# Optimization experiments

Measured on AMD Instinct MI355X. Metric: run time of the kernel, lower is better.

Reference implementation:

```python
import jax, jax.numpy as jnp
import numpy as np

Q = 10000   # num_question
D = 64      # dim_s
M = 50      # size_m
B = 64      # batch
T = 512     # seq_len


def setup_inputs() -> dict:
    key = jax.random.key(0)
    ks = jax.random.split(key, 14)
    s = 1.0 / np.sqrt(D)
    inp = {
        "question": jax.random.randint(ks[0], (B, T), 0, Q, dtype=jnp.int32),
        "response": jax.random.randint(ks[1], (B, T), 0, 2, dtype=jnp.int32),
        "mask": jnp.ones((B, T), dtype=jnp.float32),
        "k_emb": jax.random.normal(ks[2], (Q, D), jnp.float32) * s,
        "v_emb": jax.random.normal(ks[3], (2 * Q, D), jnp.float32) * s,
        "Mk": jax.random.normal(ks[4], (M, D), jnp.float32) * np.sqrt(2.0 / D),
        "Mv0": jax.random.normal(ks[5], (M, D), jnp.float32) * np.sqrt(2.0 / D),
        "e_W": jax.random.normal(ks[6], (D, D), jnp.float32) * s,
        "e_b": jnp.zeros((D,), jnp.float32),
        "a_W": jax.random.normal(ks[7], (D, D), jnp.float32) * s,
        "a_b": jnp.zeros((D,), jnp.float32),
        "f_W": jax.random.normal(ks[8], (2 * D, D), jnp.float32) * (1.0 / np.sqrt(2 * D)),
        "f_b": jnp.zeros((D,), jnp.float32),
        "p_W": jax.random.normal(ks[9], (D, 1), jnp.float32) * s,
        "p_b": jnp.zeros((1,), jnp.float32),
    }
    return inp


def reference(question, response, mask, k_emb, v_emb, Mk, Mv0,
              e_W, e_b, a_W, a_b, f_W, f_b, p_W, p_b):
    num_q = k_emb.shape[0]
    bsz = question.shape[0]
    x = question + num_q * response                      # [B,T] combined ids
    k = k_emb[question]                                  # [B,T,D]
    v = v_emb[x]                                         # [B,T,D]
    w = jax.nn.softmax(k @ Mk.T, axis=-1)                # [B,T,M] read/write weights
    e = jax.nn.sigmoid(v @ e_W + e_b)                    # [B,T,D] erase
    a = jnp.tanh(v @ a_W + a_b)                          # [B,T,D] add

    def step(Mvt, inp):
        wt, et, at, mt = inp                             # [B,M],[B,D],[B,D],[B]
        Mvn = Mvt * (1.0 - wt[:, :, None] * et[:, None, :]) + wt[:, :, None] * at[:, None, :]
        Mvt = jnp.where(mt[:, None, None] == 1, Mvn, Mvt)
        return Mvt, Mvt

    Mv0b = jnp.broadcast_to(Mv0, (bsz,) + Mv0.shape)     # [B,M,D]
    xs = (jnp.swapaxes(w, 0, 1), jnp.swapaxes(e, 0, 1),
          jnp.swapaxes(a, 0, 1), mask.T)
    _, Mv_seq = jax.lax.scan(step, Mv0b, xs)             # [T,B,M,D] states after steps 0..T-1
    # read at step t (t>=1) uses state after step t-1
    Mv_read = jnp.swapaxes(Mv_seq[:-1], 0, 1)            # [B,T-1,M,D]
    read = jnp.einsum('btm,btmd->btd', w[:, 1:], Mv_read)
    f = jnp.tanh(jnp.concatenate([read, k[:, 1:]], axis=-1) @ f_W + f_b)
    p = (f @ p_W + p_b).squeeze(-1)                      # [B,T-1]
    return p
```

## Files before the change

kernel.cpp:

```cpp
#include <hip/hip_runtime.h>
#include <cstddef>

#define QN 10000
#define DD 64
#define MM 50
#define BB 64
#define TT 512
#define WPAD 52
#define MG 25

#define PIN(arr, n)                                        \
  _Pragma("unroll") for (int _p = 0; _p < (n); ++_p)       \
      asm volatile("" : "+v"((arr)[_p]));

__global__ __launch_bounds__(256) void kPre(
    const int* __restrict__ question, const int* __restrict__ response,
    const float* __restrict__ mask,
    const float* __restrict__ k_emb, const float* __restrict__ v_emb,
    const float* __restrict__ Mk,
    const float* __restrict__ e_W, const float* __restrict__ e_b,
    const float* __restrict__ a_W, const float* __restrict__ a_b,
    float* __restrict__ w_buf, float* __restrict__ e_buf,
    float* __restrict__ a_buf) {
  const int lane = (int)(threadIdx.x & 63);
  const int wslot = __builtin_amdgcn_readfirstlane((int)(threadIdx.x >> 6));
  const int gw = blockIdx.x * 4 + wslot;
  const int NW = gridDim.x * 4;
  const int wq = (NW * 2) / 5;
  const int eq = (NW * 3) / 10;
  const int aq = NW - wq - eq;

  if (gw < wq) {
    const int idx = gw;
    const int stride4 = wq * 4;
    float mk[64];
    const int mrow = lane < MM ? lane : (MM - 1);
#pragma unroll
    for (int i = 0; i < 64; i += 4) {
      const float4 t4 = *(const float4*)(Mk + mrow * 64 + i);
      mk[i] = t4.x; mk[i + 1] = t4.y; mk[i + 2] = t4.z; mk[i + 3] = t4.w;
    }
    for (int base = idx * 4; base < BB * TT; base += stride4) {
      const int4 q4 = *(const int4*)(question + base);
      const float* __restrict__ kr0 = k_emb + (size_t)q4.x * 64;
      const float* __restrict__ kr1 = k_emb + (size_t)q4.y * 64;
      const float* __restrict__ kr2 = k_emb + (size_t)q4.z * 64;
      const float* __restrict__ kr3 = k_emb + (size_t)q4.w * 64;
      float l00=0.f,l01=0.f,l02=0.f,l03=0.f;
      float l10=0.f,l11=0.f,l12=0.f,l13=0.f;
      float l20=0.f,l21=0.f,l22=0.f,l23=0.f;
      float l30=0.f,l31=0.f,l32=0.f,l33=0.f;
#pragma unroll
      for (int i = 0; i < 64; i += 4) {
        const float4 k0 = *(const float4*)(kr0 + i);
        const float4 k1 = *(const float4*)(kr1 + i);
        const float4 k2 = *(const float4*)(kr2 + i);
        const float4 k3 = *(const float4*)(kr3 + i);
        l00 = fmaf(k0.x, mk[i], l00); l01 = fmaf(k0.y, mk[i+1], l01);
        l02 = fmaf(k0.z, mk[i+2], l02); l03 = fmaf(k0.w, mk[i+3], l03);
        l10 = fmaf(k1.x, mk[i], l10); l11 = fmaf(k1.y, mk[i+1], l11);
        l12 = fmaf(k1.z, mk[i+2], l12); l13 = fmaf(k1.w, mk[i+3], l13);
        l20 = fmaf(k2.x, mk[i], l20); l21 = fmaf(k2.y, mk[i+1], l21);
        l22 = fmaf(k2.z, mk[i+2], l22); l23 = fmaf(k2.w, mk[i+3], l23);
        l30 = fmaf(k3.x, mk[i], l30); l31 = fmaf(k3.y, mk[i+1], l31);
        l32 = fmaf(k3.z, mk[i+2], l32); l33 = fmaf(k3.w, mk[i+3], l33);
      }
      float lm[4];
      lm[0] = (l00 + l01) + (l02 + l03);
      lm[1] = (l10 + l11) + (l12 + l13);
      lm[2] = (l20 + l21) + (l22 + l23);
      lm[3] = (l30 + l31) + (l32 + l33);
#pragma unroll
      for (int r = 0; r < 4; ++r) {
        float lv = (lane < MM) ? lm[r] : -3.4e38f;
#pragma unroll
        for (int off = 32; off > 0; off >>= 1) lv = fmaxf(lv, __shfl_xor(lv, off));
        float pe = (lane < MM) ? __expf(lm[r] - lv) : 0.f;
        float ss = pe;
#pragma unroll
        for (int off = 32; off > 0; off >>= 1) ss += __shfl_xor(ss, off);
        if (lane < MM) w_buf[(size_t)(base + r) * WPAD + lane] = pe / ss;
      }
    }
  } else if (gw < wq + eq) {
    const int idx = gw - wq;
    const int stride4 = eq * 4;
    float ew[64];
#pragma unroll
    for (int i = 0; i < 64; ++i) ew[i] = e_W[i * 64 + lane];
    const float eb = e_b[lane];
    for (int base = idx * 4; base < BB * TT; base += stride4) {
      const int4 q4 = *(const int4*)(question + base);
      const int4 r4 = *(const int4*)(response + base);
      const float4 m4 = *(const float4*)(mask + base);
      const float* __restrict__ v0 = v_emb + ((size_t)q4.x + (size_t)QN * r4.x) * 64;
      const float* __restrict__ v1 = v_emb + ((size_t)q4.y + (size_t)QN * r4.y) * 64;
      const float* __restrict__ v2 = v_emb + ((size_t)q4.z + (size_t)QN * r4.z) * 64;
      const float* __restrict__ v3 = v_emb + ((size_t)q4.w + (size_t)QN * r4.w) * 64;
      float e00 = eb, e01 = 0.f, e10 = eb, e11 = 0.f;
      float e20 = eb, e21 = 0.f, e30 = eb, e31 = 0.f;
#pragma unroll
      for (int i = 0; i < 64; i += 4) {
        const float4 a0 = *(const float4*)(v0 + i);
        const float4 a1 = *(const float4*)(v1 + i);
        const float4 a2 = *(const float4*)(v2 + i);
        const float4 a3 = *(const float4*)(v3 + i);
        e00 = fmaf(a0.x, ew[i], e00);     e01 = fmaf(a0.y, ew[i + 1], e01);
        e00 = fmaf(a0.z, ew[i + 2], e00); e01 = fmaf(a0.w, ew[i + 3], e01);
        e10 = fmaf(a1.x, ew[i], e10);     e11 = fmaf(a1.y, ew[i + 1], e11);
        e10 = fmaf(a1.z, ew[i + 2], e10); e11 = fmaf(a1.w, ew[i + 3], e11);
        e20 = fmaf(a2.x, ew[i], e20);     e21 = fmaf(a2.y, ew[i + 1], e21);
        e20 = fmaf(a2.z, ew[i + 2], e20); e21 = fmaf(a2.w, ew[i + 3], e21);
        e30 = fmaf(a3.x, ew[i], e30);     e31 = fmaf(a3.y, ew[i + 1], e31);
        e30 = fmaf(a3.z, ew[i + 2], e30); e31 = fmaf(a3.w, ew[i + 3], e31);
      }
      const float mf0 = (m4.x == 1.0f) ? 1.0f : 0.0f;
      const float mf1 = (m4.y == 1.0f) ? 1.0f : 0.0f;
      const float mf2 = (m4.z == 1.0f) ? 1.0f : 0.0f;
      const float mf3 = (m4.w == 1.0f) ? 1.0f : 0.0f;
      e_buf[(size_t)(base + 0) * 64 + lane] = mf0 / (1.f + __expf(-(e00 + e01)));
      e_buf[(size_t)(base + 1) * 64 + lane] = mf1 / (1.f + __expf(-(e10 + e11)));
      e_buf[(size_t)(base + 2) * 64 + lane] = mf2 / (1.f + __expf(-(e20 + e21)));
      e_buf[(size_t)(base + 3) * 64 + lane] = mf3 / (1.f + __expf(-(e30 + e31)));
    }
  } else {
    const int idx = gw - wq - eq;
    const int stride4 = aq * 4;
    float aw[64];
#pragma unroll
    for (int i = 0; i < 64; ++i) aw[i] = a_W[i * 64 + lane];
    const float ab = a_b[lane];
    for (int base = idx * 4; base < BB * TT; base += stride4) {
      const int4 q4 = *(const int4*)(question + base);
      const int4 r4 = *(const int4*)(response + base);
      const float4 m4 = *(const float4*)(mask + base);
      const float* __restrict__ v0 = v_emb + ((size_t)q4.x + (size_t)QN * r4.x) * 64;
      const float* __restrict__ v1 = v_emb + ((size_t)q4.y + (size_t)QN * r4.y) * 64;
      const float* __restrict__ v2 = v_emb + ((size_t)q4.z + (size_t)QN * r4.z) * 64;
      const float* __restrict__ v3 = v_emb + ((size_t)q4.w + (size_t)QN * r4.w) * 64;
      float a00 = ab, a01 = 0.f, a10 = ab, a11 = 0.f;
      float a20 = ab, a21 = 0.f, a30 = ab, a31 = 0.f;
#pragma unroll
      for (int i = 0; i < 64; i += 4) {
        const float4 x0 = *(const float4*)(v0 + i);
        const float4 x1 = *(const float4*)(v1 + i);
        const float4 x2 = *(const float4*)(v2 + i);
        const float4 x3 = *(const float4*)(v3 + i);
        a00 = fmaf(x0.x, aw[i], a00);     a01 = fmaf(x0.y, aw[i + 1], a01);
        a00 = fmaf(x0.z, aw[i + 2], a00); a01 = fmaf(x0.w, aw[i + 3], a01);
        a10 = fmaf(x1.x, aw[i], a10);     a11 = fmaf(x1.y, aw[i + 1], a11);
        a10 = fmaf(x1.z, aw[i + 2], a10); a11 = fmaf(x1.w, aw[i + 3], a11);
        a20 = fmaf(x2.x, aw[i], a20);     a21 = fmaf(x2.y, aw[i + 1], a21);
        a20 = fmaf(x2.z, aw[i + 2], a20); a21 = fmaf(x2.w, aw[i + 3], a21);
        a30 = fmaf(x3.x, aw[i], a30);     a31 = fmaf(x3.y, aw[i + 1], a31);
        a30 = fmaf(x3.z, aw[i + 2], a30); a31 = fmaf(x3.w, aw[i + 3], a31);
      }
      const float mf0 = (m4.x == 1.0f) ? 1.0f : 0.0f;
      const float mf1 = (m4.y == 1.0f) ? 1.0f : 0.0f;
      const float mf2 = (m4.z == 1.0f) ? 1.0f : 0.0f;
      const float mf3 = (m4.w == 1.0f) ? 1.0f : 0.0f;
      const float s0 = a00 + a01, s1 = a10 + a11, s2 = a20 + a21, s3 = a30 + a31;
      a_buf[(size_t)(base + 0) * 64 + lane] = mf0 * (1.f - 2.f / (__expf(2.f * s0) + 1.f));
      a_buf[(size_t)(base + 1) * 64 + lane] = mf1 * (1.f - 2.f / (__expf(2.f * s1) + 1.f));
      a_buf[(size_t)(base + 2) * 64 + lane] = mf2 * (1.f - 2.f / (__expf(2.f * s2) + 1.f));
      a_buf[(size_t)(base + 3) * 64 + lane] = mf3 * (1.f - 2.f / (__expf(2.f * s3) + 1.f));
    }
  }
}

#define STAGE_W(wl_row, rowbase)                                            \
  {                                                                         \
    const float* __restrict__ wsrc = w_buf + (rowbase) * WPAD;              \
    _Pragma("unroll") for (int k = 0; k < 13; ++k) {                        \
      const int idx = lane + k * 64;                            \
      const int row = idx / 52;                                             \
      const int col = idx - row * 52;                                       \
      (wl_row)[row * 56 + col + (col >= 25 ? 3 : 0)] = wsrc[idx];           \
    }                                                                       \
  }

#define LOAD_WM(wm, wl_row, j, g)                                           \
  const float* __restrict__ wj_##j = (wl_row) + (j) * 56 + (g) * 28;        \
  const float4 q0_##j = *(const float4*)(wj_##j + 0);                       \
  const float4 q1_##j = *(const float4*)(wj_##j + 4);                       \
  const float4 q2_##j = *(const float4*)(wj_##j + 8);                       \
  const float4 q3_##j = *(const float4*)(wj_##j + 12);                      \
  const float4 q4_##j = *(const float4*)(wj_##j + 16);                      \
  const float4 q5_##j = *(const float4*)(wj_##j + 20);                      \
  const float4 q6_##j = *(const float4*)(wj_##j + 24);                      \
  const float wm[MG] = {q0_##j.x, q0_##j.y, q0_##j.z, q0_##j.w,             \
                        q1_##j.x, q1_##j.y, q1_##j.z, q1_##j.w,             \
                        q2_##j.x, q2_##j.y, q2_##j.z, q2_##j.w,             \
                        q3_##j.x, q3_##j.y, q3_##j.z, q3_##j.w,             \
                        q4_##j.x, q4_##j.y, q4_##j.z, q4_##j.w,             \
                        q5_##j.x, q5_##j.y, q5_##j.z, q5_##j.w, q6_##j.x};

__global__ __launch_bounds__(256) void kA16(
    const float* __restrict__ w_buf, const float* __restrict__ e_buf,
    const float* __restrict__ a_buf, float* __restrict__ AB) {
  __shared__ float wl[4][16 * 56];
  const int lane = (int)(threadIdx.x & 63);
  const int wslot = __builtin_amdgcn_readfirstlane((int)(threadIdx.x >> 6));
  const int u2 = blockIdx.x * 4 + wslot;
  if (u2 >= BB * 32 * 2) return;
  const int g = u2 & 1;
  const int unit = u2 >> 1;
  const int b = unit >> 5;
  const int c = unit & 31;
  const size_t rowbase = (size_t)b * TT + c * 16;
  const size_t eb0 = rowbase * 64 + lane;

  float ev[16], av[16];
#pragma unroll
  for (int j = 0; j < 16; ++j) {
    ev[j] = e_buf[eb0 + (size_t)j * 64];
    av[j] = a_buf[eb0 + (size_t)j * 64];
  }
  STAGE_W(wl[wslot], rowbase)

  float Am[MG], Bm[MG];
#pragma unroll
  for (int m = 0; m < MG; ++m) { Am[m] = 1.f; Bm[m] = 0.f; }

#pragma unroll
  for (int j = 0; j < 16; ++j) {
    LOAD_WM(wm, wl[wslot], j, g)
#pragma unroll
    for (int m = 0; m < MG; ++m) {
      const float al = fmaf(-wm[m], ev[j], 1.0f);
      const float be = wm[m] * av[j];
      Am[m] *= al;
      Bm[m] = fmaf(Bm[m], al, be);
    }
  }
  float* __restrict__ abp = AB + (size_t)unit * 6400 + (g * MG) * 128 + lane * 2;
#pragma unroll
  for (int m = 0; m < MG; ++m) {
    float2 o; o.x = Am[m]; o.y = Bm[m];
    *(float2*)(abp + m * 128) = o;
  }
}

__global__ __launch_bounds__(256) void kB_entry(
    const float* __restrict__ AB, const float* __restrict__ Mv0,
    float* __restrict__ entry, int C) {
  const int NT = gridDim.x * 256;
  for (int idx = blockIdx.x * 256 + (int)threadIdx.x; idx < BB * MM * 64;
       idx += NT) {
    const int b = idx / (MM * 64);
    const int r = idx - b * (MM * 64);
    float s = Mv0[r];
    const float* __restrict__ abp = AB + (size_t)b * C * 6400 + (size_t)r * 2;
    float* __restrict__ ep = entry + (size_t)b * C * 3200 + r;
    if (C == 32) {
      float2 ab[32];
#pragma unroll
      for (int c = 0; c < 32; ++c)
        ab[c] = *(const float2*)(abp + (size_t)c * 6400);
#pragma unroll
      for (int c = 0; c < 32; ++c) {
        ep[(size_t)c * 3200] = s;
        s = fmaf(ab[c].x, s, ab[c].y);
      }
    } else {
      float2 cur = *(const float2*)(abp);
      for (int c = 0; c < C; ++c) {
        ep[(size_t)c * 3200] = s;
        float2 nxt; nxt.x = 1.f; nxt.y = 0.f;
        if (c + 1 < C) nxt = *(const float2*)(abp + (size_t)(c + 1) * 6400);
        s = fmaf(cur.x, s, cur.y);
        cur = nxt;
      }
    }
  }
}

__global__ __launch_bounds__(256) void kC16sum(
    const float* __restrict__ w_buf, const float* __restrict__ e_buf,
    const float* __restrict__ a_buf, const float* __restrict__ entry,
    float* __restrict__ read_buf) {
  __shared__ float wl[4][16 * 56];
  __shared__ float p_lds[4][16][64];
  const int lane = (int)(threadIdx.x & 63);
  const int wslot = __builtin_amdgcn_readfirstlane((int)(threadIdx.x >> 6));
  const int u2 = blockIdx.x * 4 + wslot;
  const int g = u2 & 1;
  const int unit = u2 >> 1;
  const int b = unit >> 5;
  const int c = unit & 31;
  const size_t rowbase = (size_t)b * TT + c * 16;
  const size_t eb0 = rowbase * 64 + lane;

  float ev[16], av[16];
#pragma unroll
  for (int j = 0; j < 16; ++j) {
    ev[j] = e_buf[eb0 + (size_t)j * 64];
    av[j] = a_buf[eb0 + (size_t)j * 64];
  }
  float s[MG];
  {
    const float* __restrict__ ep =
        entry + (size_t)unit * 3200 + (g * MG) * 64 + lane;
#pragma unroll
    for (int m = 0; m < MG; ++m) s[m] = ep[m * 64];
  }
  STAGE_W(wl[wslot], rowbase)

#pragma unroll
  for (int j = 0; j < 16; ++j) {
    LOAD_WM(wm, wl[wslot], j, g)
    float a0 = 0.f, a1 = 0.f;
#pragma unroll
    for (int m = 0; m < MG - 1; m += 2) {
      a0 = fmaf(wm[m], s[m], a0);
      a1 = fmaf(wm[m + 1], s[m + 1], a1);
    }
    a0 = fmaf(wm[MG - 1], s[MG - 1], a0);
    p_lds[wslot][j][lane] = a0 + a1;
#pragma unroll
    for (int m = 0; m < MG; ++m)
      s[m] = fmaf(wm[m], fmaf(-s[m], ev[j], av[j]), s[m]);
  }
  __syncthreads();

  {
    const int p = wslot >> 1;
    const int uown = blockIdx.x * 2 + p;
    const int ob = uown >> 5;
    const int oc = uown & 31;
    const int t0 = oc * 16;
    const int j0 = (oc == 0 && g == 0) ? 1 : g * 8;
    const int j1 = g * 8 + 8;
    for (int j = j0; j < j1; ++j) {
      const int t = t0 + j;
      const float r = p_lds[2 * p][j][lane] + p_lds[2 * p + 1][j][lane];
      read_buf[((size_t)ob * (TT - 1) + (t - 1)) * 64 + lane] = r;
    }
  }
}

__global__ __launch_bounds__(256) void kA_chunk(
    const float* __restrict__ w_buf, const float* __restrict__ e_buf,
    const float* __restrict__ a_buf, float* __restrict__ AB, int logC, int L) {
  const int lane = (int)(threadIdx.x & 63);
  const int wslot = __builtin_amdgcn_readfirstlane((int)(threadIdx.x >> 6));
  const int NW = gridDim.x * 4;
  const int C = 1 << logC;
  for (int u2 = blockIdx.x * 4 + wslot; u2 < BB * C * 2; u2 += NW) {
    const int g = u2 & 1;
    const int unit = u2 >> 1;
    const int b = unit >> logC;
    const int c = unit & (C - 1);
    float Am[MG], Bm[MG];
#pragma unroll
    for (int m = 0; m < MG; ++m) { Am[m] = 1.f; Bm[m] = 0.f; }
    const size_t rowbase = (size_t)b * TT + c * L;
#pragma unroll 2
    for (int j = 0; j < L; ++j) {
      const size_t row = rowbase + j;
      const float ed = e_buf[row * 64 + lane];
      const float ad = a_buf[row * 64 + lane];
      const float* __restrict__ wr = w_buf + row * WPAD + g * MG;
#pragma unroll
      for (int m = 0; m < MG; ++m) {
        const float wm = wr[m];
        const float al = fmaf(-wm, ed, 1.0f);
        const float be = wm * ad;
        Am[m] *= al;
        Bm[m] = fmaf(Bm[m], al, be);
      }
    }
    float* __restrict__ abp = AB + (size_t)unit * 6400 + (g * MG) * 128 + lane * 2;
#pragma unroll
    for (int m = 0; m < MG; ++m) {
      float2 o; o.x = Am[m]; o.y = Bm[m];
      *(float2*)(abp + m * 128) = o;
    }
  }
}

__global__ __launch_bounds__(256) void kC_read(
    const float* __restrict__ w_buf, const float* __restrict__ e_buf,
    const float* __restrict__ a_buf, const float* __restrict__ entry,
    const float* __restrict__ Mv0, float* __restrict__ read2,
    int logC, int L, int use_mv0) {
  const int lane = (int)(threadIdx.x & 63);
  const int wslot = __builtin_amdgcn_readfirstlane((int)(threadIdx.x >> 6));
  const int NW = gridDim.x * 4;
  const int C = 1 << logC;
  const size_t RN = (size_t)BB * (TT - 1) * 64;
  for (int u2 = blockIdx.x * 4 + wslot; u2 < BB * C * 2; u2 += NW) {
    const int g = u2 & 1;
    const int unit = u2 >> 1;
    const int b = unit >> logC;
    const int c = unit & (C - 1);
    float s[MG];
    if (use_mv0) {
#pragma unroll
      for (int m = 0; m < MG; ++m) s[m] = Mv0[(g * MG + m) * 64 + lane];
    } else {
      const float* __restrict__ ep =
          entry + (size_t)unit * 3200 + (g * MG) * 64 + lane;
#pragma unroll
      for (int m = 0; m < MG; ++m) s[m] = ep[m * 64];
    }
    const int t0 = c * L;
    float* __restrict__ rb = read2 + (size_t)g * RN;
    for (int j = 0; j < L; ++j) {
      const int t = t0 + j;
      const size_t row = (size_t)b * TT + t;
      const float ed = e_buf[row * 64 + lane];
      const float ad = a_buf[row * 64 + lane];
      const float* __restrict__ wr = w_buf + row * WPAD + g * MG;
      if (t >= 1) {
        float a0 = 0.f, a1 = 0.f;
#pragma unroll
        for (int m = 0; m < MG - 1; m += 2) {
          a0 = fmaf(wr[m], s[m], a0);
          a1 = fmaf(wr[m + 1], s[m + 1], a1);
        }
        a0 = fmaf(wr[MG - 1], s[MG - 1], a0);
        rb[((size_t)b * (TT - 1) + (t - 1)) * 64 + lane] = a0 + a1;
      }
#pragma unroll
      for (int m = 0; m < MG; ++m)
        s[m] = fmaf(wr[m], fmaf(-s[m], ed, ad), s[m]);
    }
  }
}

__global__ __launch_bounds__(256) void k3_out(
    const int* __restrict__ question, const float* __restrict__ k_emb,
    const float* __restrict__ read_buf,
    const float* __restrict__ f_W, const float* __restrict__ f_b,
    const float* __restrict__ p_W, const float* __restrict__ p_b,
    float* __restrict__ out) {
  __shared__ float pbuf[2][2][64];
  __shared__ float stg[4][64];
  const int lane = (int)(threadIdx.x & 63);
  const int ws = __builtin_amdgcn_readfirstlane((int)(threadIdx.x >> 6));
  const int pair = ws >> 1;
  const int g = ws & 1;
  const int NP = gridDim.x * 2;
  const int R = BB * (TT - 1);
  const int iters = (R + NP - 1) / NP;

  float fw[64];
#pragma unroll
  for (int i = 0; i < 64; ++i) fw[i] = f_W[(g * 64 + i) * 64 + lane];
  PIN(fw, 64)
  const float fb = f_b[lane];
  const float pw = p_W[lane];
  const float pb = p_b[0];

  int row = blockIdx.x * 2 + pair;
  float cur = 0.f;
  if (row < R) {
    if (g == 0) {
      cur = read_buf[(size_t)row * 64 + lane];
    } else {
      const int b = row / (TT - 1);
      const int tp = row - b * (TT - 1);
      const int qn = question[b * TT + tp + 1];
      cur = k_emb[(size_t)qn * 64 + lane];
    }
  }
  for (int it = 0; it < iters; ++it) {
    const int nrow = row + NP;
    float nxt = 0.f;
    if (nrow < R) {
      if (g == 0) {
        nxt = read_buf[(size_t)nrow * 64 + lane];
      } else {
        const int nb = nrow / (TT - 1);
        const int ntp = nrow - nb * (TT - 1);
        const int nqn = question[nb * TT + ntp + 1];
        nxt = k_emb[(size_t)nqn * 64 + lane];
      }
    }
    const bool active = (row < R);
    float partial = 0.f;
    if (active) {
      stg[ws][lane] = cur;
      float f0 = (g == 0) ? fb : 0.f, f1 = 0.f, f2 = 0.f, f3 = 0.f;
#pragma unroll
      for (int i = 0; i < 64; i += 4) {
        const float4 xv = *(const float4*)&stg[ws][i];
        f0 = fmaf(xv.x, fw[i], f0);
        f1 = fmaf(xv.y, fw[i + 1], f1);
        f2 = fmaf(xv.z, fw[i + 2], f2);
        f3 = fmaf(xv.w, fw[i + 3], f3);
      }
      partial = (f0 + f1) + (f2 + f3);
    }
    const int pr = it & 1;
    if (active && g == 1) pbuf[pr][pair][lane] = partial;
    __syncthreads();
    if (active && g == 0) {
      const float f = partial + pbuf[pr][pair][lane];
      const float t2 = __expf(2.f * f);
      const float fv = 1.f - 2.f / (t2 + 1.f);
      float acc = fv * pw;
#pragma unroll
      for (int off = 32; off > 0; off >>= 1) acc += __shfl_xor(acc, off);
      if (lane == 0) out[row] = acc + pb;
    }
    row = nrow; cur = nxt;
  }
}

__global__ __launch_bounds__(256) void k3_out2(
    const int* __restrict__ question, const float* __restrict__ k_emb,
    const float* __restrict__ read2,
    const float* __restrict__ f_W, const float* __restrict__ f_b,
    const float* __restrict__ p_W, const float* __restrict__ p_b,
    float* __restrict__ out) {
  __shared__ float pbuf[2][2][64];
  __shared__ float stg[4][64];
  const int lane = (int)(threadIdx.x & 63);
  const int ws = __builtin_amdgcn_readfirstlane((int)(threadIdx.x >> 6));
  const int pair = ws >> 1;
  const int g = ws & 1;
  const int NP = gridDim.x * 2;
  const size_t RN = (size_t)BB * (TT - 1) * 64;
  const int R = BB * (TT - 1);
  const int iters = (R + NP - 1) / NP;

  float fw[64];
#pragma unroll
  for (int i = 0; i < 64; ++i) fw[i] = f_W[(g * 64 + i) * 64 + lane];
  PIN(fw, 64)
  const float fb = f_b[lane];
  const float pw = p_W[lane];
  const float pb = p_b[0];

  int row = blockIdx.x * 2 + pair;
  float cur = 0.f;
  if (row < R) {
    if (g == 0) {
      cur = read2[(size_t)row * 64 + lane] + read2[RN + (size_t)row * 64 + lane];
    } else {
      const int b = row / (TT - 1);
      const int tp = row - b * (TT - 1);
      const int qn = question[b * TT + tp + 1];
      cur = k_emb[(size_t)qn * 64 + lane];
    }
  }
  for (int it = 0; it < iters; ++it) {
    const int nrow = row + NP;
    float nxt = 0.f;
    if (nrow < R) {
      if (g == 0) {
        nxt = read2[(size_t)nrow * 64 + lane] +
              read2[RN + (size_t)nrow * 64 + lane];
      } else {
        const int nb = nrow / (TT - 1);
        const int ntp = nrow - nb * (TT - 1);
        const int nqn = question[nb * TT + ntp + 1];
        nxt = k_emb[(size_t)nqn * 64 + lane];
      }
    }
    const bool active = (row < R);
    float partial = 0.f;
    if (active) {
      stg[ws][lane] = cur;
      float f0 = (g == 0) ? fb : 0.f, f1 = 0.f, f2 = 0.f, f3 = 0.f;
#pragma unroll
      for (int i = 0; i < 64; i += 4) {
        const float4 xv = *(const float4*)&stg[ws][i];
        f0 = fmaf(xv.x, fw[i], f0);
        f1 = fmaf(xv.y, fw[i + 1], f1);
        f2 = fmaf(xv.z, fw[i + 2], f2);
        f3 = fmaf(xv.w, fw[i + 3], f3);
      }
      partial = (f0 + f1) + (f2 + f3);
    }
    const int pr = it & 1;
    if (active && g == 1) pbuf[pr][pair][lane] = partial;
    __syncthreads();
    if (active && g == 0) {
      const float f = partial + pbuf[pr][pair][lane];
      const float t2 = __expf(2.f * f);
      const float fv = 1.f - 2.f / (t2 + 1.f);
      float acc = fv * pw;
#pragma unroll
      for (int off = 32; off > 0; off >>= 1) acc += __shfl_xor(acc, off);
      if (lane == 0) out[row] = acc + pb;
    }
    row = nrow; cur = nxt;
  }
}

extern "C" void kernel_launch(void* const* d_in, const int* in_sizes, int n_in,
                              void* d_out, int out_size, void* d_ws, size_t ws_size,
                              hipStream_t stream) {
  const int*   question = (const int*)d_in[0];
  const int*   response = (const int*)d_in[1];
  const float* mask     = (const float*)d_in[2];
  const float* k_emb    = (const float*)d_in[3];
  const float* v_emb    = (const float*)d_in[4];
  const float* Mk       = (const float*)d_in[5];
  const float* Mv0      = (const float*)d_in[6];
  const float* e_W      = (const float*)d_in[7];
  const float* e_b      = (const float*)d_in[8];
  const float* a_W      = (const float*)d_in[9];
  const float* a_b      = (const float*)d_in[10];
  const float* f_W      = (const float*)d_in[11];
  const float* f_b      = (const float*)d_in[12];
  const float* p_W      = (const float*)d_in[13];
  const float* p_b      = (const float*)d_in[14];
  float* out = (float*)d_out;

  const size_t wN  = (size_t)BB * TT * WPAD;
  const size_t eN  = (size_t)BB * TT * 64;
  const size_t r2N = 2ull * BB * (TT - 1) * 64;
  float* ws = (float*)d_ws;
  float* w_buf  = ws;
  float* e_buf  = w_buf + wN;
  float* a_buf  = e_buf + eN;
  float* readws = a_buf + eN;
  float* AB_arr = readws + r2N;
  const size_t baseN = wN + 2 * eN + r2N;

  int C = 32, logC = 5;
  while (C >= 2) {
    const size_t need = (baseN + 9600ull * BB * C) * sizeof(float);
    if (need <= ws_size) break;
    C >>= 1; logC -= 1;
  }
  int useChunks = (C >= 2);
  if (!useChunks) { C = 1; logC = 0; }
  const int L = TT / C;
  float* entry = AB_arr + 6400ull * BB * C;

  hipLaunchKernelGGL(kPre, dim3(2048), dim3(256), 0, stream,
                     question, response, mask, k_emb, v_emb, Mk,
                     e_W, e_b, a_W, a_b, w_buf, e_buf, a_buf);

  if (C == 32) {
    hipLaunchKernelGGL(kA16, dim3(1024), dim3(256), 0, stream,
                       w_buf, e_buf, a_buf, AB_arr);
    hipLaunchKernelGGL(kB_entry, dim3((BB * MM * 64 + 255) / 256), dim3(256),
                       0, stream, AB_arr, Mv0, entry, C);
    hipLaunchKernelGGL(kC16sum, dim3(1024), dim3(256), 0, stream,
                       w_buf, e_buf, a_buf, entry, readws);
    hipLaunchKernelGGL(k3_out, dim3(1024), dim3(256), 0, stream,
                       question, k_emb, readws, f_W, f_b, p_W, p_b, out);
  } else {
    if (useChunks) {
      const int ublocksA = (BB * C * 2 + 3) / 4;
      hipLaunchKernelGGL(kA_chunk, dim3(ublocksA), dim3(256), 0, stream,
                         w_buf, e_buf, a_buf, AB_arr, logC, L);
      hipLaunchKernelGGL(kB_entry, dim3((BB * MM * 64 + 255) / 256), dim3(256),
                         0, stream, AB_arr, Mv0, entry, C);
    }
    const int ublocksC = (BB * C * 2 + 3) / 4;
    hipLaunchKernelGGL(kC_read, dim3(ublocksC), dim3(256), 0, stream,
                       w_buf, e_buf, a_buf, entry, Mv0, readws,
                       logC, L, useChunks ? 0 : 1);
    hipLaunchKernelGGL(k3_out2, dim3(1024), dim3(256), 0, stream,
                       question, k_emb, readws, f_W, f_b, p_W, p_b, out);
  }
}
```

Measured before the change: 181.2 us.

## Fuse chunk read kernel with output projection to drop read buffer round-trip

Merges the per-chunk memory-read kernel and the output MLP kernel into one kernel for the C==32 path. Read vectors stay in LDS and feed the f_W/p_W projection directly, so the read buffer is never written to or read back from global memory, and one kernel launch is removed. In exchange, each block now loads the 64-register f_W slice and runs 16 serialized steps with a block barrier each, which raises register pressure and may lower occupancy.

```diff
diff --git a/kernel.cpp b/kernel.cpp
--- a/kernel.cpp
+++ b/kernel.cpp
@@ -275,12 +275,18 @@
   }
 }
 
-__global__ __launch_bounds__(256) void kC16sum(
+__global__ __launch_bounds__(256) void kCD2(
+    const int* __restrict__ question,
     const float* __restrict__ w_buf, const float* __restrict__ e_buf,
     const float* __restrict__ a_buf, const float* __restrict__ entry,
-    float* __restrict__ read_buf) {
+    const float* __restrict__ k_emb,
+    const float* __restrict__ f_W, const float* __restrict__ f_b,
+    const float* __restrict__ p_W, const float* __restrict__ p_b,
+    float* __restrict__ out) {
   __shared__ float wl[4][16 * 56];
   __shared__ float p_lds[4][16][64];
+  __shared__ float pbuf[2][2][64];
+  __shared__ float stg[4][64];
   const int lane = (int)(threadIdx.x & 63);
   const int wslot = __builtin_amdgcn_readfirstlane((int)(threadIdx.x >> 6));
   const int u2 = blockIdx.x * 4 + wslot;
@@ -291,50 +297,91 @@
   const size_t rowbase = (size_t)b * TT + c * 16;
   const size_t eb0 = rowbase * 64 + lane;
 
-  float ev[16], av[16];
-#pragma unroll
-  for (int j = 0; j < 16; ++j) {
-    ev[j] = e_buf[eb0 + (size_t)j * 64];
-    av[j] = a_buf[eb0 + (size_t)j * 64];
-  }
-  float s[MG];
   {
+    float ev[16], av[16];
+#pragma unroll
+    for (int j = 0; j < 16; ++j) {
+      ev[j] = e_buf[eb0 + (size_t)j * 64];
+      av[j] = a_buf[eb0 + (size_t)j * 64];
+    }
+    float s[MG];
     const float* __restrict__ ep =
         entry + (size_t)unit * 3200 + (g * MG) * 64 + lane;
 #pragma unroll
     for (int m = 0; m < MG; ++m) s[m] = ep[m * 64];
-  }
-  STAGE_W(wl[wslot], rowbase)
-
-#pragma unroll
+    STAGE_W(wl[wslot], rowbase)
+
+#pragma unroll
+    for (int j = 0; j < 16; ++j) {
+      LOAD_WM(wm, wl[wslot], j, g)
+      float a0 = 0.f, a1 = 0.f;
+#pragma unroll
+      for (int m = 0; m < MG - 1; m += 2) {
+        a0 = fmaf(wm[m], s[m], a0);
+        a1 = fmaf(wm[m + 1], s[m + 1], a1);
+      }
+      a0 = fmaf(wm[MG - 1], s[MG - 1], a0);
+      p_lds[wslot][j][lane] = a0 + a1;
+#pragma unroll
+      for (int m = 0; m < MG; ++m)
+        s[m] = fmaf(wm[m], fmaf(-s[m], ev[j], av[j]), s[m]);
+    }
+  }
+  __syncthreads();
+
+  const int p = wslot >> 1;
+  const int uown = blockIdx.x * 2 + p;
+  const int ob = uown >> 5;
+  const int oc = uown & 31;
+  const int t0 = oc * 16;
+
+  float fw[64];
+#pragma unroll
+  for (int i = 0; i < 64; ++i) fw[i] = f_W[(g * 64 + i) * 64 + lane];
+  PIN(fw, 64)
+  const float fb = f_b[lane];
+  const float pw = p_W[lane];
+  const float pb = p_b[0];
+
+  float nxt_k = 0.f;
+  if (g == 1) {
+    const int qn = question[(size_t)ob * TT + t0];
+    nxt_k = k_emb[(size_t)qn * 64 + lane];
+  }
   for (int j = 0; j < 16; ++j) {
-    LOAD_WM(wm, wl[wslot], j, g)
-    float a0 = 0.f, a1 = 0.f;
-#pragma unroll
-    for (int m = 0; m < MG - 1; m += 2) {
-      a0 = fmaf(wm[m], s[m], a0);
-      a1 = fmaf(wm[m + 1], s[m + 1], a1);
-    }
-    a0 = fmaf(wm[MG - 1], s[MG - 1], a0);
-    p_lds[wslot][j][lane] = a0 + a1;
-#pragma unroll
-    for (int m = 0; m < MG; ++m)
-      s[m] = fmaf(wm[m], fmaf(-s[m], ev[j], av[j]), s[m]);
-  }
-  __syncthreads();
-
-  {
-    const int p = wslot >> 1;
-    const int uown = blockIdx.x * 2 + p;
-    const int ob = uown >> 5;
-    const int oc = uown & 31;
-    const int t0 = oc * 16;
-    const int j0 = (oc == 0 && g == 0) ? 1 : g * 8;
-    const int j1 = g * 8 + 8;
-    for (int j = j0; j < j1; ++j) {
-      const int t = t0 + j;
-      const float r = p_lds[2 * p][j][lane] + p_lds[2 * p + 1][j][lane];
-      read_buf[((size_t)ob * (TT - 1) + (t - 1)) * 64 + lane] = r;
+    const int t = t0 + j;
+    float cur;
+    if (g == 0) {
+      cur = p_lds[2 * p][j][lane] + p_lds[2 * p + 1][j][lane];
+    } else {
+      cur = nxt_k;
+      if (j + 1 < 16) {
+        const int qn = question[(size_t)ob * TT + t + 1];
+        nxt_k = k_emb[(size_t)qn * 64 + lane];
+      }
+    }
+    stg[wslot][lane] = cur;
+    float f0 = (g == 0) ? fb : 0.f, f1 = 0.f, f2 = 0.f, f3 = 0.f;
+#pragma unroll
+    for (int i = 0; i < 64; i += 4) {
+      const float4 xv = *(const float4*)&stg[wslot][i];
+      f0 = fmaf(xv.x, fw[i], f0);
+      f1 = fmaf(xv.y, fw[i + 1], f1);
+      f2 = fmaf(xv.z, fw[i + 2], f2);
+      f3 = fmaf(xv.w, fw[i + 3], f3);
+    }
+    const float partial = (f0 + f1) + (f2 + f3);
+    const int pr = j & 1;
+    if (g == 1) pbuf[pr][p][lane] = partial;
+    __syncthreads();
+    if (g == 0 && t >= 1) {
+      const float f = partial + pbuf[pr][p][lane];
+      const float t2 = __expf(2.f * f);
+      const float fv = 1.f - 2.f / (t2 + 1.f);
+      float acc = fv * pw;
+#pragma unroll
+      for (int off = 32; off > 0; off >>= 1) acc += __shfl_xor(acc, off);
+      if (lane == 0) out[(size_t)ob * (TT - 1) + (t - 1)] = acc + pb;
     }
   }
 }
@@ -426,86 +473,6 @@
       for (int m = 0; m < MG; ++m)
         s[m] = fmaf(wr[m], fmaf(-s[m], ed, ad), s[m]);
     }
-  }
-}
-
-__global__ __launch_bounds__(256) void k3_out(
-    const int* __restrict__ question, const float* __restrict__ k_emb,
-    const float* __restrict__ read_buf,
-    const float* __restrict__ f_W, const float* __restrict__ f_b,
-    const float* __restrict__ p_W, const float* __restrict__ p_b,
-    float* __restrict__ out) {
-  __shared__ float pbuf[2][2][64];
-  __shared__ float stg[4][64];
-  const int lane = (int)(threadIdx.x & 63);
-  const int ws = __builtin_amdgcn_readfirstlane((int)(threadIdx.x >> 6));
-  const int pair = ws >> 1;
-  const int g = ws & 1;
-  const int NP = gridDim.x * 2;
-  const int R = BB * (TT - 1);
-  const int iters = (R + NP - 1) / NP;
-
-  float fw[64];
-#pragma unroll
-  for (int i = 0; i < 64; ++i) fw[i] = f_W[(g * 64 + i) * 64 + lane];
-  PIN(fw, 64)
-  const float fb = f_b[lane];
-  const float pw = p_W[lane];
-  const float pb = p_b[0];
-
-  int row = blockIdx.x * 2 + pair;
-  float cur = 0.f;
-  if (row < R) {
-    if (g == 0) {
-      cur = read_buf[(size_t)row * 64 + lane];
-    } else {
-      const int b = row / (TT - 1);
-      const int tp = row - b * (TT - 1);
-      const int qn = question[b * TT + tp + 1];
-      cur = k_emb[(size_t)qn * 64 + lane];
-    }
-  }
-  for (int it = 0; it < iters; ++it) {
-    const int nrow = row + NP;
-    float nxt = 0.f;
-    if (nrow < R) {
-      if (g == 0) {
-        nxt = read_buf[(size_t)nrow * 64 + lane];
-      } else {
-        const int nb = nrow / (TT - 1);
-        const int ntp = nrow - nb * (TT - 1);
-        const int nqn = question[nb * TT + ntp + 1];
-        nxt = k_emb[(size_t)nqn * 64 + lane];
-      }
-    }
-    const bool active = (row < R);
-    float partial = 0.f;
-    if (active) {
-      stg[ws][lane] = cur;
-      float f0 = (g == 0) ? fb : 0.f, f1 = 0.f, f2 = 0.f, f3 = 0.f;
-#pragma unroll
-      for (int i = 0; i < 64; i += 4) {
-        const float4 xv = *(const float4*)&stg[ws][i];
-        f0 = fmaf(xv.x, fw[i], f0);
-        f1 = fmaf(xv.y, fw[i + 1], f1);
-        f2 = fmaf(xv.z, fw[i + 2], f2);
-        f3 = fmaf(xv.w, fw[i + 3], f3);
-      }
-      partial = (f0 + f1) + (f2 + f3);
-    }
-    const int pr = it & 1;
-    if (active && g == 1) pbuf[pr][pair][lane] = partial;
-    __syncthreads();
-    if (active && g == 0) {
-      const float f = partial + pbuf[pr][pair][lane];
-      const float t2 = __expf(2.f * f);
-      const float fv = 1.f - 2.f / (t2 + 1.f);
-      float acc = fv * pw;
-#pragma unroll
-      for (int off = 32; off > 0; off >>= 1) acc += __shfl_xor(acc, off);
-      if (lane == 0) out[row] = acc + pb;
-    }
-    row = nrow; cur = nxt;
   }
 }
 
@@ -642,10 +609,9 @@
                        w_buf, e_buf, a_buf, AB_arr);
     hipLaunchKernelGGL(kB_entry, dim3((BB * MM * 64 + 255) / 256), dim3(256),
                        0, stream, AB_arr, Mv0, entry, C);
-    hipLaunchKernelGGL(kC16sum, dim3(1024), dim3(256), 0, stream,
-                       w_buf, e_buf, a_buf, entry, readws);
-    hipLaunchKernelGGL(k3_out, dim3(1024), dim3(256), 0, stream,
-                       question, k_emb, readws, f_W, f_b, p_W, p_b, out);
+    hipLaunchKernelGGL(kCD2, dim3(1024), dim3(256), 0, stream,
+                       question, w_buf, e_buf, a_buf, entry, k_emb,
+                       f_W, f_b, p_W, p_b, out);
   } else {
     if (useChunks) {
       const int ublocksA = (BB * C * 2 + 3) / 4;
```

After: 173.2 us (median of 2 runs). -4.4%, faster.
